# Optimization experiments

Hardware: AMD Instinct MI355X
Metric: run time of the kernel (lower is better)

## Reference

```python
import jax, jax.numpy as jnp
import numpy as np

NUM_HEADS = 12
HEAD_DIM = 64
SO3_DIM = 30  # round(64*0.5)//3*3
ROPE_FREQ = 100.0


def _rope1d(t, p):
    # t: [B,H,N,Dh], p: [B,N]
    half = t.shape[-1] // 2
    inv = 1.0 / (ROPE_FREQ ** (jnp.arange(half, dtype=jnp.float32) / half))
    ang = p[:, None, :, None] * inv  # [B,1,N,half]
    cos = jnp.concatenate([jnp.cos(ang)] * 2, axis=-1)
    sin = jnp.concatenate([jnp.sin(ang)] * 2, axis=-1)
    t1, t2 = t[..., :half], t[..., half:]
    return t * cos + jnp.concatenate([-t2, t1], axis=-1) * sin


def _rope2d(x, pos):
    # x: [B,H,N,D], pos: [B,N,2] (y,x)
    Dh = x.shape[-1] // 2
    return jnp.concatenate([
        _rope1d(x[..., :Dh], pos[..., 0]),
        _rope1d(x[..., Dh:], pos[..., 1]),
    ], axis=-1)


def _so3prope(t, R, num_img):
    # t: [B,H,S,Nt,Dh], R: [B,S,3,3]; rotate first SO3_DIM channels of the
    # first num_img (image) tokens as 3-vectors; special tokens untouched.
    img, sp = t[..., :num_img, :], t[..., num_img:, :]
    B, H, S, Ni, D = img.shape
    v = img[..., :SO3_DIM].reshape(B, H, S, Ni, SO3_DIM // 3, 3)
    v = jnp.einsum('bsij,bhsnkj->bhsnki', R, v).reshape(B, H, S, Ni, SO3_DIM)
    img = jnp.concatenate([v, img[..., SO3_DIM:]], axis=-1)
    return jnp.concatenate([img, sp], axis=-2)


def setup_inputs() -> dict:
    key = jax.random.key(0)
    ks = jax.random.split(key, 6)
    B, HW, S, Nt, C = 1, 576, 4, 577, 768
    G = 24  # 24x24 patch grid
    q_tokens = jax.random.normal(ks[0], (B, HW, C), dtype=jnp.float32)
    t_tokens = jax.random.normal(ks[1], (B, S, Nt, C), dtype=jnp.float32)
    yy, xx = jnp.meshgrid(jnp.arange(G, dtype=jnp.float32), jnp.arange(G, dtype=jnp.float32), indexing='ij')
    pos2d = jnp.broadcast_to(jnp.stack([yy, xx], axis=-1).reshape(1, HW, 2), (B, HW, 2))
    # random proper rotations via QR
    A = jax.random.normal(ks[2], (B, S, 3, 3), dtype=jnp.float32)
    Q, _ = jnp.linalg.qr(A)
    poses = jnp.tile(jnp.eye(4, dtype=jnp.float32), (B, S, 1, 1))
    template_poses = poses.at[:, :, :3, :3].set(Q)
    W_qkv = jax.random.normal(ks[3], (C, 3 * C), dtype=jnp.float32) * 0.02
    b_qkv = jnp.zeros((3 * C,), dtype=jnp.float32)
    W_proj = jax.random.normal(ks[4], (C, C), dtype=jnp.float32) * 0.02
    b_proj = jnp.zeros((C,), dtype=jnp.float32)
    return {'q_tokens': q_tokens, 't_tokens': t_tokens, 'pos2d': pos2d,
            'template_poses': template_poses, 'W_qkv': W_qkv, 'b_qkv': b_qkv,
            'W_proj': W_proj, 'b_proj': b_proj}


def reference(q_tokens, t_tokens, pos2d, template_poses, W_qkv, b_qkv, W_proj, b_proj):
    B, HW, C = q_tokens.shape
    S, Nt = t_tokens.shape[1], t_tokens.shape[2]
    x = jnp.concatenate([q_tokens, t_tokens.reshape(B, S * Nt, C)], axis=1)  # [B,N,C]
    N = x.shape[1]
    qkv = (x @ W_qkv + b_qkv).reshape(B, N, 3, NUM_HEADS, HEAD_DIM)
    q = jnp.transpose(qkv[:, :, 0], (0, 2, 1, 3))  # [B,H,N,d]
    k = jnp.transpose(qkv[:, :, 1], (0, 2, 1, 3))
    v = jnp.transpose(qkv[:, :, 2], (0, 2, 1, 3))
    # RoPE2D on query-image tokens only
    q = jnp.concatenate([_rope2d(q[:, :, :HW], pos2d), q[:, :, HW:]], axis=2)
    k = jnp.concatenate([_rope2d(k[:, :, :HW], pos2d), k[:, :, HW:]], axis=2)
    # SO3Prope on template image tokens
    R = template_poses[:, :, :3, :3]
    q_t = _so3prope(q[:, :, HW:].reshape(B, NUM_HEADS, S, Nt, HEAD_DIM), R, HW)
    k_t = _so3prope(k[:, :, HW:].reshape(B, NUM_HEADS, S, Nt, HEAD_DIM), R, HW)
    q = jnp.concatenate([q[:, :, :HW], q_t.reshape(B, NUM_HEADS, S * Nt, HEAD_DIM)], axis=2)
    k = jnp.concatenate([k[:, :, :HW], k_t.reshape(B, NUM_HEADS, S * Nt, HEAD_DIM)], axis=2)
    # SDPA (no mask, no dropout at eval)
    scale = HEAD_DIM ** -0.5
    attn = jax.nn.softmax(jnp.einsum('bhnd,bhmd->bhnm', q, k) * scale, axis=-1)
    out = jnp.einsum('bhnm,bhmd->bhnd', attn, v)
    out = jnp.transpose(out, (0, 2, 1, 3)).reshape(B, N, C)
    out = out @ W_proj + b_proj
    return out[:, :HW, :], out[:, HW:, :].reshape(B, S, Nt, C)
```

## Files before the change

### kernel.cpp

```cpp
#include <hip/hip_runtime.h>
#include <hip/hip_bf16.h>
#include <hip/hip_fp16.h>
#include <math.h>

#define N_TOK 2884
#define HW_IMG 576
#define NT_TOK 577
#define CDIM 768
#define NH 12
#define HD 64
#define QKV_COLS 2304
#define NVP 2944
#define NQT 46
#define LOG2E 1.44269504088896340736f

typedef float f32x4 __attribute__((ext_vector_type(4)));
typedef short bf16x8 __attribute__((ext_vector_type(8)));
typedef _Float16 f16x8 __attribute__((ext_vector_type(8)));
typedef unsigned short u16;
typedef unsigned short u16x8 __attribute__((ext_vector_type(8)));
typedef unsigned short u16x4 __attribute__((ext_vector_type(4)));

static __device__ __forceinline__ u16 f2bf(float f) {
    union { __hip_bfloat16 b; u16 u; } cv;
    cv.b = __float2bfloat16(f);
    return cv.u;
}
static __device__ __forceinline__ float bf2f(u16 h) {
    return __uint_as_float(((unsigned)h) << 16);
}
static __device__ __forceinline__ void split1(float f, u16& h, u16& l) {
    h = f2bf(f);
    l = f2bf(f - bf2f(h));
}
static __device__ __forceinline__ f16x8 as_f16x8(u16x8 u) {
    union { u16x8 u; f16x8 h; } c; c.u = u; return c.h;
}

__global__ __launch_bounds__(256)
void conv_x(const float* __restrict__ q, const float* __restrict__ t,
            u16* __restrict__ Xhi, u16* __restrict__ Xlo)
{
    const int i = (blockIdx.x * 256 + threadIdx.x) * 4;
    const int SPLIT = HW_IMG * CDIM;
    const float4 v = (i < SPLIT) ? *(const float4*)(q + i) : *(const float4*)(t + (i - SPLIT));
    u16x4 h, l;
    u16 hh, ll;
    split1(v.x, hh, ll); h[0] = hh; l[0] = ll;
    split1(v.y, hh, ll); h[1] = hh; l[1] = ll;
    split1(v.z, hh, ll); h[2] = hh; l[2] = ll;
    split1(v.w, hh, ll); h[3] = hh; l[3] = ll;
    *(u16x4*)(Xhi + i) = h;
    *(u16x4*)(Xlo + i) = l;
}

__global__ __launch_bounds__(256)
void conv_wT(const float* __restrict__ W, int ncols,
             u16* __restrict__ Thi, u16* __restrict__ Tlo)
{
    __shared__ float T[64][65];
    const int k0 = blockIdx.x * 64;
    const int n0 = blockIdx.y * 64;
    const int tid = threadIdx.x;
    {
        const int kr = tid >> 2, nch = (tid & 3) << 4;
        const float* src = W + (size_t)(k0 + kr) * ncols + n0 + nch;
        #pragma unroll
        for (int c = 0; c < 4; ++c) {
            const float4 f = *(const float4*)(src + c * 4);
            T[kr][nch + c * 4 + 0] = f.x;
            T[kr][nch + c * 4 + 1] = f.y;
            T[kr][nch + c * 4 + 2] = f.z;
            T[kr][nch + c * 4 + 3] = f.w;
        }
    }
    __syncthreads();
    const int nr = tid >> 2, kch = (tid & 3) << 4;
    u16x8 h0, h1, l0v, l1v;
    #pragma unroll
    for (int j = 0; j < 8; ++j) { u16 hh, ll; split1(T[kch + j][nr], hh, ll); h0[j] = hh; l0v[j] = ll; }
    #pragma unroll
    for (int j = 0; j < 8; ++j) { u16 hh, ll; split1(T[kch + 8 + j][nr], hh, ll); h1[j] = hh; l1v[j] = ll; }
    const size_t dst = (size_t)(n0 + nr) * CDIM + k0 + kch;
    *(u16x8*)(Thi + dst) = h0;     *(u16x8*)(Thi + dst + 8) = h1;
    *(u16x8*)(Tlo + dst) = l0v;    *(u16x8*)(Tlo + dst + 8) = l1v;
}

__global__ __launch_bounds__(256, 3)
void qkv_mfma(const u16* __restrict__ Xhi, const u16* __restrict__ Xlo,
              const u16* __restrict__ Whi, const u16* __restrict__ Wlo,
              const float* __restrict__ bqkv,
              const float* __restrict__ pos2d, const float* __restrict__ tposes,
              u16* __restrict__ Qhi, u16* __restrict__ Qlo,
              u16* __restrict__ Khi, u16* __restrict__ Klo,
              u16* __restrict__ Vthi)
{
    __shared__ __align__(16) char smem[49152];
    u16 (*Ah)[64] = (u16(*)[64])(smem);
    u16 (*Al)[64] = (u16(*)[64])(smem + 16384);
    u16 (*Bh)[64] = (u16(*)[64])(smem + 32768);
    u16 (*Bl)[64] = (u16(*)[64])(smem + 40960);
    float (*Ct)[65] = (float(*)[65])(smem);

    const int rb = blockIdx.x;
    const int cb = blockIdx.y;
    const int which = cb / NH;
    const int h = cb - which * NH;
    const int colbase = cb * 64;
    const int tid = threadIdx.x;
    const int w = tid >> 6, l = tid & 63;
    const int lr = l & 15, lg = l >> 4;

    const int sa_r = tid >> 1;
    const int sa_c = (tid & 1) << 5;
    int arow = rb * 128 + sa_r;
    if (arow >= N_TOK) arow = N_TOK - 1;
    const size_t abase = (size_t)arow * CDIM + sa_c;
    const int swa_ = (sa_r & 7) << 3;
    const int sb_r = tid >> 2;
    const int sb_c = (tid & 3) << 4;
    const size_t bbase = (size_t)(colbase + sb_r) * CDIM + sb_c;
    const int swb_ = (sb_r & 7) << 3;

    const int swf = (lr & 7) << 3;

    f32x4 acc[2][4];
    #pragma unroll
    for (int rf = 0; rf < 2; ++rf)
        #pragma unroll
        for (int i = 0; i < 4; ++i) acc[rf][i] = (f32x4){0.f, 0.f, 0.f, 0.f};

    for (int k0 = 0; k0 < CDIM; k0 += 64) {
        u16x8 a_h[4], a_l[4], b_h[2], b_l[2];
        #pragma unroll
        for (int c = 0; c < 4; ++c) {
            a_h[c] = *(const u16x8*)(Xhi + abase + k0 + c * 8);
            a_l[c] = *(const u16x8*)(Xlo + abase + k0 + c * 8);
        }
        #pragma unroll
        for (int c = 0; c < 2; ++c) {
            b_h[c] = *(const u16x8*)(Whi + bbase + k0 + c * 8);
            b_l[c] = *(const u16x8*)(Wlo + bbase + k0 + c * 8);
        }
        __syncthreads();
        #pragma unroll
        for (int c = 0; c < 4; ++c) {
            *(u16x8*)&Ah[sa_r][(sa_c + c * 8) ^ swa_] = a_h[c];
            *(u16x8*)&Al[sa_r][(sa_c + c * 8) ^ swa_] = a_l[c];
        }
        #pragma unroll
        for (int c = 0; c < 2; ++c) {
            *(u16x8*)&Bh[sb_r][(sb_c + c * 8) ^ swb_] = b_h[c];
            *(u16x8*)&Bl[sb_r][(sb_c + c * 8) ^ swb_] = b_l[c];
        }
        __syncthreads();
        #pragma unroll
        for (int ks = 0; ks < 2; ++ks) {
            const int koff = (ks * 32 + lg * 8) ^ swf;
            const bf16x8 ah0 = *(const bf16x8*)&Ah[w * 32 + lr][koff];
            const bf16x8 al0 = *(const bf16x8*)&Al[w * 32 + lr][koff];
            const bf16x8 ah1 = *(const bf16x8*)&Ah[w * 32 + 16 + lr][koff];
            const bf16x8 al1 = *(const bf16x8*)&Al[w * 32 + 16 + lr][koff];
            #pragma unroll
            for (int cbk = 0; cbk < 4; ++cbk) {
                const bf16x8 bh_ = *(const bf16x8*)&Bh[cbk * 16 + lr][koff];
                const bf16x8 bl_ = *(const bf16x8*)&Bl[cbk * 16 + lr][koff];
                acc[0][cbk] = __builtin_amdgcn_mfma_f32_16x16x32_bf16(ah0, bh_, acc[0][cbk], 0, 0, 0);
                acc[0][cbk] = __builtin_amdgcn_mfma_f32_16x16x32_bf16(ah0, bl_, acc[0][cbk], 0, 0, 0);
                acc[0][cbk] = __builtin_amdgcn_mfma_f32_16x16x32_bf16(al0, bh_, acc[0][cbk], 0, 0, 0);
                acc[1][cbk] = __builtin_amdgcn_mfma_f32_16x16x32_bf16(ah1, bh_, acc[1][cbk], 0, 0, 0);
                acc[1][cbk] = __builtin_amdgcn_mfma_f32_16x16x32_bf16(ah1, bl_, acc[1][cbk], 0, 0, 0);
                acc[1][cbk] = __builtin_amdgcn_mfma_f32_16x16x32_bf16(al1, bh_, acc[1][cbk], 0, 0, 0);
            }
        }
    }

    __syncthreads();
    #pragma unroll
    for (int rf = 0; rf < 2; ++rf)
        #pragma unroll
        for (int cbk = 0; cbk < 4; ++cbk)
            #pragma unroll
            for (int r = 0; r < 4; ++r)
                Ct[w * 32 + rf * 16 + lg * 4 + r][cbk * 16 + lr] =
                    acc[rf][cbk][r] + bqkv[colbase + cbk * 16 + lr];
    __syncthreads();

    if (which < 2) {
        #pragma unroll
        for (int it = 0; it < 2; ++it) {
            const int item = it * 256 + tid;
            const int er = item >> 2;
            const int eu = item & 3;
            const int n = rb * 128 + er;
            if (n < N_TOK) {
                float outv[16];
                const bool is_img = (n < HW_IMG);
                int ts = 0, tj = 0;
                if (!is_img) { const int m = n - HW_IMG; ts = m / NT_TOK; tj = m - ts * NT_TOK; }

                if (is_img) {
                    const float p = (eu < 2) ? pos2d[2 * n] : pos2d[2 * n + 1];
                    const bool lowhalf = ((eu & 1) == 0);
                    #pragma unroll
                    for (int dd = 0; dd < 16; ++dd) {
                        const int d = (eu << 4) + dd;
                        float sv, cv;
                        sincosf(p * expf((float)dd * -0.28782313662425574f), &sv, &cv);
                        const float rot = lowhalf ? -Ct[er][d + 16] : Ct[er][d - 16];
                        outv[dd] = Ct[er][d] * cv + rot * sv;
                    }
                } else if (tj < HW_IMG) {
                    #pragma unroll
                    for (int dd = 0; dd < 16; ++dd) {
                        const int d = (eu << 4) + dd;
                        float val = Ct[er][d];
                        if (d < 30) {
                            const int g = d / 3;
                            const float* R = tposes + ts * 16 + (d - g * 3) * 4;
                            val = R[0] * Ct[er][g * 3] + R[1] * Ct[er][g * 3 + 1] + R[2] * Ct[er][g * 3 + 2];
                        }
                        outv[dd] = val;
                    }
                } else {
                    #pragma unroll
                    for (int dd = 0; dd < 16; ++dd) outv[dd] = Ct[er][(eu << 4) + dd];
                }

                const float scale = (which == 0) ? (0.125f * LOG2E) : 1.0f;
                u16x8 h0, h1, l0v, l1v;
                #pragma unroll
                for (int j = 0; j < 8; ++j) { u16 hh, ll; split1(outv[j] * scale, hh, ll); h0[j] = hh; l0v[j] = ll; }
                #pragma unroll
                for (int j = 0; j < 8; ++j) { u16 hh, ll; split1(outv[8 + j] * scale, hh, ll); h1[j] = hh; l1v[j] = ll; }
                u16* dh = (which == 0 ? Qhi : Khi) + ((size_t)h * N_TOK + n) * HD + (eu << 4);
                u16* dl = (which == 0 ? Qlo : Klo) + ((size_t)h * N_TOK + n) * HD + (eu << 4);
                *(u16x8*)dh = h0;  *(u16x8*)(dh + 8) = h1;
                *(u16x8*)dl = l0v; *(u16x8*)(dl + 8) = l1v;
            }
        }
    } else {
        #pragma unroll
        for (int it = 0; it < 2; ++it) {
            const int item = it * 256 + tid;
            const int vd_ = item >> 3;
            const int vch = (item & 7) << 4;
            const int tokbase = rb * 128 + vch;
            u16 th[16];
            #pragma unroll
            for (int j = 0; j < 16; ++j)
                th[j] = (tokbase + j < N_TOK)
                      ? __half_as_ushort(__float2half(Ct[vch + j][vd_]))
                      : (u16)0;
            u16* dh = Vthi + (size_t)(h * HD + vd_) * NVP + tokbase;
            *(u16x8*)dh = *(u16x8*)&th[0];
            *(u16x8*)(dh + 8) = *(u16x8*)&th[8];
        }
    }
}

__global__ __launch_bounds__(256, 3)
void attn_shard(const u16* __restrict__ Qhi, const u16* __restrict__ Qlo,
                const u16* __restrict__ Khi, const u16* __restrict__ Klo,
                const u16* __restrict__ Vthi,
                float* __restrict__ Pacc, float2* __restrict__ PmL,
                int TS, int SPLITS)
{
    __shared__ __align__(16) u16 Kh_s[64][64], Kl_s[64][64];
    __shared__ __align__(16) u16 Vh_s[64][64];
    __shared__ __align__(16) u16 P2[64][64];

    int qb, head, sh;
    {
        const int flat = blockIdx.x + NQT * (blockIdx.y + NH * blockIdx.z);
        if (SPLITS == 4) {
            const int grp = flat & 7;
            const int rest = flat >> 3;
            qb = rest % NQT;
            const int hs = grp + 8 * (rest / NQT);
            head = hs % NH;
            sh = hs / NH;
        } else {
            qb = blockIdx.x; head = blockIdx.y; sh = blockIdx.z;
        }
    }
    const int tid = threadIdx.x;
    const int w = tid >> 6, l = tid & 63;
    const int lr = l & 15, lg = l >> 4;

    const int kt_begin = sh * TS;
    const int kt_end = min(NQT, kt_begin + TS);

    bf16x8 qh_[2], ql_[2];
    {
        int row = qb * 64 + w * 16 + lr;
        if (row >= N_TOK) row = N_TOK - 1;
        const u16* qph = Qhi + ((size_t)head * N_TOK + row) * HD;
        const u16* qpl = Qlo + ((size_t)head * N_TOK + row) * HD;
        #pragma unroll
        for (int ks = 0; ks < 2; ++ks) {
            qh_[ks] = *(const bf16x8*)(qph + ks * 32 + lg * 8);
            ql_[ks] = *(const bf16x8*)(qpl + ks * 32 + lg * 8);
        }
    }

    float m0[4] = {-1e30f, -1e30f, -1e30f, -1e30f};
    float l0[4] = {0.f, 0.f, 0.f, 0.f};
    f32x4 acc[4];
    #pragma unroll
    for (int db = 0; db < 4; ++db) acc[db] = (f32x4){0.f, 0.f, 0.f, 0.f};

    const int skey = tid >> 2, sch = (tid & 3) << 4;
    const int vd_ = tid >> 2, vch = (tid & 3) << 4;
    const int swk = (skey & 7) << 3;
    const int swv = (vd_ & 7) << 3;
    const int swf = (lr & 7) << 3;
    const u16* KhH = Khi + (size_t)head * N_TOK * HD;
    const u16* KlH = Klo + (size_t)head * N_TOK * HD;
    const size_t vrowbase = (size_t)(head * HD + vd_) * NVP;

    u16x8 rk0h, rk1h, rk0l, rk1l, rv0h, rv1h;
    auto LOADT = [&](int kt) {
        const int kbase = kt << 6;
        int krow = kbase + skey;
        if (krow >= N_TOK) krow = N_TOK - 1;
        const u16* kph = KhH + (size_t)krow * HD + sch;
        const u16* kpl = KlH + (size_t)krow * HD + sch;
        rk0h = *(const u16x8*)kph;  rk1h = *(const u16x8*)(kph + 8);
        rk0l = *(const u16x8*)kpl;  rk1l = *(const u16x8*)(kpl + 8);
        const u16* vph = Vthi + vrowbase + kbase + vch;
        rv0h = *(const u16x8*)vph;  rv1h = *(const u16x8*)(vph + 8);
    };
    LOADT(kt_begin);

    for (int kt = kt_begin; kt < kt_end; ++kt) {
        const int kbase = kt << 6;

        __syncthreads();
        *(u16x8*)&Kh_s[skey][(sch + 0) ^ swk] = rk0h;
        *(u16x8*)&Kh_s[skey][(sch + 8) ^ swk] = rk1h;
        *(u16x8*)&Kl_s[skey][(sch + 0) ^ swk] = rk0l;
        *(u16x8*)&Kl_s[skey][(sch + 8) ^ swk] = rk1l;
        *(u16x8*)&Vh_s[vd_][(vch + 0) ^ swv] = rv0h;
        *(u16x8*)&Vh_s[vd_][(vch + 8) ^ swv] = rv1h;
        if (kt + 1 < kt_end) LOADT(kt + 1);
        __syncthreads();

        f32x4 s[4];
        __builtin_amdgcn_s_setprio(1);
        #pragma unroll
        for (int kb = 0; kb < 4; ++kb) {
            s[kb] = (f32x4){0.f, 0.f, 0.f, 0.f};
            const int key = kb * 16 + lr;
            #pragma unroll
            for (int ks = 0; ks < 2; ++ks) {
                const int koff = (ks * 32 + lg * 8) ^ swf;
                const bf16x8 bh = *(const bf16x8*)&Kh_s[key][koff];
                const bf16x8 bl = *(const bf16x8*)&Kl_s[key][koff];
                s[kb] = __builtin_amdgcn_mfma_f32_16x16x32_bf16(qh_[ks], bh, s[kb], 0, 0, 0);
                s[kb] = __builtin_amdgcn_mfma_f32_16x16x32_bf16(qh_[ks], bl, s[kb], 0, 0, 0);
                s[kb] = __builtin_amdgcn_mfma_f32_16x16x32_bf16(ql_[ks], bh, s[kb], 0, 0, 0);
            }
        }
        __builtin_amdgcn_s_setprio(0);

        if (kbase + 64 > N_TOK) {
            #pragma unroll
            for (int kb = 0; kb < 4; ++kb)
                if (kbase + kb * 16 + lr >= N_TOK) {
                    #pragma unroll
                    for (int r = 0; r < 4; ++r) s[kb][r] = -1e30f;
                }
        }

        float mt[4];
        #pragma unroll
        for (int r = 0; r < 4; ++r)
            mt[r] = fmaxf(fmaxf(s[0][r], s[1][r]), fmaxf(s[2][r], s[3][r]));
        #pragma unroll
        for (int r = 0; r < 4; ++r) {
            mt[r] = fmaxf(mt[r], __shfl_xor(mt[r], 1));
            mt[r] = fmaxf(mt[r], __shfl_xor(mt[r], 2));
            mt[r] = fmaxf(mt[r], __shfl_xor(mt[r], 4));
            mt[r] = fmaxf(mt[r], __shfl_xor(mt[r], 8));
        }
        const bool newmax = __any((mt[0] > m0[0]) | (mt[1] > m0[1]) |
                                  (mt[2] > m0[2]) | (mt[3] > m0[3]));
        if (newmax) {
            float al[4];
            #pragma unroll
            for (int r = 0; r < 4; ++r) {
                const float mn = fmaxf(m0[r], mt[r]);
                al[r] = __builtin_amdgcn_exp2f(m0[r] - mn);
                m0[r] = mn;
            }
            #pragma unroll
            for (int r = 0; r < 4; ++r) l0[r] *= al[r];
            #pragma unroll
            for (int db = 0; db < 4; ++db)
                #pragma unroll
                for (int r = 0; r < 4; ++r) acc[db][r] *= al[r];
        }
        #pragma unroll
        for (int kb = 0; kb < 4; ++kb)
            #pragma unroll
            for (int r = 0; r < 4; ++r)
                s[kb][r] = __builtin_amdgcn_exp2f(s[kb][r] - m0[r]);
        #pragma unroll
        for (int r = 0; r < 4; ++r)
            l0[r] += s[0][r] + s[1][r] + s[2][r] + s[3][r];

        #pragma unroll
        for (int r = 0; r < 4; ++r) {
            const int rw = w * 16 + lg * 4 + r;
            const int swp = (rw & 7) << 3;
            #pragma unroll
            for (int kb = 0; kb < 4; ++kb)
                P2[rw][(kb * 16 + lr) ^ swp] = __half_as_ushort(__float2half(s[kb][r]));
        }

        const int arow = w * 16 + lr;
        const int swpa = (arow & 7) << 3;
        #pragma unroll
        for (int ks = 0; ks < 2; ++ks) {
            const int kb8 = ks * 32 + lg * 8;
            const f16x8 pa = as_f16x8(*(const u16x8*)&P2[arow][kb8 ^ swpa]);
            __builtin_amdgcn_s_setprio(1);
            #pragma unroll
            for (int db = 0; db < 4; ++db) {
                const int vr = db * 16 + lr;
                const f16x8 vh = as_f16x8(*(const u16x8*)&Vh_s[vr][kb8 ^ swf]);
                acc[db] = __builtin_amdgcn_mfma_f32_16x16x32_f16(pa, vh, acc[db], 0, 0, 0);
            }
            __builtin_amdgcn_s_setprio(0);
        }
    }

    #pragma unroll
    for (int r = 0; r < 4; ++r) {
        l0[r] += __shfl_xor(l0[r], 1);
        l0[r] += __shfl_xor(l0[r], 2);
        l0[r] += __shfl_xor(l0[r], 4);
        l0[r] += __shfl_xor(l0[r], 8);
    }
    const size_t pb = (((size_t)sh * NH + head) * NQT + qb) << 6;
    float* pout = Pacc + (pb << 6);
    #pragma unroll
    for (int r = 0; r < 4; ++r) {
        const int lrow = w * 16 + lg * 4 + r;
        #pragma unroll
        for (int db = 0; db < 4; ++db)
            pout[(size_t)lrow * 64 + db * 16 + lr] = acc[db][r];
        if (lr == 0)
            PmL[pb + lrow] = make_float2(m0[r], l0[r]);
    }
}

__global__ __launch_bounds__(256)
void attn_combine(const float* __restrict__ Pacc, const float2* __restrict__ PmL,
                  u16* __restrict__ Ohi, u16* __restrict__ Olo, int SPLITS)
{
    const int qb = blockIdx.x, h = blockIdx.y;
    const int tid = threadIdx.x;
    const int er = tid >> 2, eu = tid & 3;
    const int row = qb * 64 + er;
    if (row >= N_TOK) return;

    float ms[4], ls[4];
    float m = -1e30f;
    for (int s = 0; s < SPLITS; ++s) {
        const float2 p = PmL[((((size_t)s * NH + h) * NQT + qb) << 6) + er];
        ms[s] = p.x; ls[s] = p.y;
        m = fmaxf(m, p.x);
    }
    float L = 0.f, Ws[4];
    for (int s = 0; s < SPLITS; ++s) { Ws[s] = __builtin_amdgcn_exp2f(ms[s] - m); L += ls[s] * Ws[s]; }
    const float inv = 1.f / L;

    float o[16];
    #pragma unroll
    for (int j = 0; j < 16; ++j) o[j] = 0.f;
    for (int s = 0; s < SPLITS; ++s) {
        const float* src = Pacc + ((((((size_t)s * NH + h) * NQT + qb) << 6) + er) << 6) + (eu << 4);
        const float wgt = Ws[s];
        #pragma unroll
        for (int c = 0; c < 4; ++c) {
            const float4 f = *(const float4*)(src + c * 4);
            o[c * 4 + 0] += wgt * f.x;
            o[c * 4 + 1] += wgt * f.y;
            o[c * 4 + 2] += wgt * f.z;
            o[c * 4 + 3] += wgt * f.w;
        }
    }
    u16x8 h0, h1, l0v, l1v;
    #pragma unroll
    for (int j = 0; j < 8; ++j) { u16 hh, ll; split1(o[j] * inv, hh, ll); h0[j] = hh; l0v[j] = ll; }
    #pragma unroll
    for (int j = 0; j < 8; ++j) { u16 hh, ll; split1(o[8 + j] * inv, hh, ll); h1[j] = hh; l1v[j] = ll; }
    u16* dh = Ohi + (size_t)row * CDIM + h * HD + (eu << 4);
    u16* dl = Olo + (size_t)row * CDIM + h * HD + (eu << 4);
    *(u16x8*)dh = h0;  *(u16x8*)(dh + 8) = h1;
    *(u16x8*)dl = l0v; *(u16x8*)(dl + 8) = l1v;
}

__global__ __launch_bounds__(256)
void proj_mfma(const u16* __restrict__ Ahi, const u16* __restrict__ Alo,
               const u16* __restrict__ Whi, const u16* __restrict__ Wlo,
               const float* __restrict__ bp, float* __restrict__ out)
{
    __shared__ __align__(16) u16 Ah[64][64], Al[64][64], Bh[64][64], Bl[64][64];

    const int rb = blockIdx.x;
    const int colbase = blockIdx.y * 64;
    const int tid = threadIdx.x;
    const int w = tid >> 6, l = tid & 63;
    const int lr = l & 15, lg = l >> 4;

    const int srow = tid >> 2, sch = (tid & 3) << 4;
    int arow = rb * 64 + srow;
    if (arow >= N_TOK) arow = N_TOK - 1;
    const size_t abase = (size_t)arow * CDIM + sch;
    const size_t bbase = (size_t)(colbase + srow) * CDIM + sch;

    f32x4 acc[4];
    #pragma unroll
    for (int i = 0; i < 4; ++i) acc[i] = (f32x4){0.f, 0.f, 0.f, 0.f};

    const int sw = (srow & 7) << 3;
    const int swf = (lr & 7) << 3;

    for (int k0 = 0; k0 < CDIM; k0 += 64) {
        const u16x8 a0h = *(const u16x8*)(Ahi + abase + k0);
        const u16x8 a1h = *(const u16x8*)(Ahi + abase + k0 + 8);
        const u16x8 a0l = *(const u16x8*)(Alo + abase + k0);
        const u16x8 a1l = *(const u16x8*)(Alo + abase + k0 + 8);
        const u16x8 b0h = *(const u16x8*)(Whi + bbase + k0);
        const u16x8 b1h = *(const u16x8*)(Whi + bbase + k0 + 8);
        const u16x8 b0l = *(const u16x8*)(Wlo + bbase + k0);
        const u16x8 b1l = *(const u16x8*)(Wlo + bbase + k0 + 8);
        __syncthreads();
        *(u16x8*)&Ah[srow][(sch + 0) ^ sw] = a0h;
        *(u16x8*)&Ah[srow][(sch + 8) ^ sw] = a1h;
        *(u16x8*)&Al[srow][(sch + 0) ^ sw] = a0l;
        *(u16x8*)&Al[srow][(sch + 8) ^ sw] = a1l;
        *(u16x8*)&Bh[srow][(sch + 0) ^ sw] = b0h;
        *(u16x8*)&Bh[srow][(sch + 8) ^ sw] = b1h;
        *(u16x8*)&Bl[srow][(sch + 0) ^ sw] = b0l;
        *(u16x8*)&Bl[srow][(sch + 8) ^ sw] = b1l;
        __syncthreads();
        #pragma unroll
        for (int ks = 0; ks < 2; ++ks) {
            const int koff = (ks * 32 + lg * 8) ^ swf;
            const bf16x8 ah_ = *(const bf16x8*)&Ah[w * 16 + lr][koff];
            const bf16x8 al_ = *(const bf16x8*)&Al[w * 16 + lr][koff];
            #pragma unroll
            for (int cbk = 0; cbk < 4; ++cbk) {
                const bf16x8 bh_ = *(const bf16x8*)&Bh[cbk * 16 + lr][koff];
                const bf16x8 bl_ = *(const bf16x8*)&Bl[cbk * 16 + lr][koff];
                acc[cbk] = __builtin_amdgcn_mfma_f32_16x16x32_bf16(ah_, bh_, acc[cbk], 0, 0, 0);
                acc[cbk] = __builtin_amdgcn_mfma_f32_16x16x32_bf16(ah_, bl_, acc[cbk], 0, 0, 0);
                acc[cbk] = __builtin_amdgcn_mfma_f32_16x16x32_bf16(al_, bh_, acc[cbk], 0, 0, 0);
            }
        }
    }

    #pragma unroll
    for (int cbk = 0; cbk < 4; ++cbk) {
        const float bb = bp[colbase + cbk * 16 + lr];
        #pragma unroll
        for (int r = 0; r < 4; ++r) {
            const int row = rb * 64 + w * 16 + lg * 4 + r;
            if (row < N_TOK)
                out[(size_t)row * CDIM + colbase + cbk * 16 + lr] = acc[cbk][r] + bb;
        }
    }
}

extern "C" void kernel_launch(void* const* d_in, const int* in_sizes, int n_in,
                              void* d_out, int out_size, void* d_ws, size_t ws_size,
                              hipStream_t stream)
{
    const float* q_tokens = (const float*)d_in[0];
    const float* t_tokens = (const float*)d_in[1];
    const float* pos2d    = (const float*)d_in[2];
    const float* tposes   = (const float*)d_in[3];
    const float* Wqkv     = (const float*)d_in[4];
    const float* bqkv     = (const float*)d_in[5];
    const float* Wproj    = (const float*)d_in[6];
    const float* bproj    = (const float*)d_in[7];
    float* out = (float*)d_out;

    const size_t PQ = (size_t)NH * N_TOK * HD;
    const size_t PV_ = (size_t)NH * HD * NVP;
    const size_t PX = (size_t)N_TOK * CDIM;
    const size_t PW = (size_t)QKV_COLS * CDIM;

    u16* base = (u16*)d_ws;
    u16* Qhi  = base;
    u16* Qlo  = Qhi + PQ;
    u16* Khi  = Qlo + PQ;
    u16* Klo  = Khi + PQ;
    u16* Vthi = Klo + PQ;
    u16* XOhi = Vthi + PV_;
    u16* XOlo = XOhi + PX;
    u16* WThi = XOlo + PX;
    u16* WTlo = WThi + PW;
    u16* planes_end = WTlo + PW;

    const size_t planes_bytes = (size_t)(planes_end - base) * sizeof(u16);
    const size_t accElems = (size_t)NH * NQT * 64 * 64;
    const size_t mlElems  = (size_t)NH * NQT * 64;
    const size_t per_shard = accElems * 4 + mlElems * 8;

    int SPLITS = 1;
    for (int cand = 4; cand >= 2; --cand) {
        if (planes_bytes + (size_t)cand * per_shard <= ws_size) { SPLITS = cand; break; }
    }
    float* Pacc = (float*)((char*)d_ws + planes_bytes);
    float2* PmL = (float2*)(Pacc + (size_t)SPLITS * accElems);
    const int TS = (NQT + SPLITS - 1) / SPLITS;

    conv_x<<<dim3((N_TOK * CDIM / 4 + 255) / 256), 256, 0, stream>>>(q_tokens, t_tokens, XOhi, XOlo);
    conv_wT<<<dim3(CDIM / 64, QKV_COLS / 64), 256, 0, stream>>>(Wqkv, QKV_COLS, WThi, WTlo);

    dim3 g1((N_TOK + 127) / 128, 36);
    qkv_mfma<<<g1, 256, 0, stream>>>(XOhi, XOlo, WThi, WTlo, bqkv, pos2d, tposes,
                                     Qhi, Qlo, Khi, Klo, Vthi);

    conv_wT<<<dim3(CDIM / 64, CDIM / 64), 256, 0, stream>>>(Wproj, CDIM, WThi, WTlo);

    dim3 g2(NQT, NH, SPLITS);
    attn_shard<<<g2, 256, 0, stream>>>(Qhi, Qlo, Khi, Klo, Vthi, Pacc, PmL, TS, SPLITS);

    dim3 g2b(NQT, NH);
    attn_combine<<<g2b, 256, 0, stream>>>(Pacc, PmL, XOhi, XOlo, SPLITS);

    dim3 g3((N_TOK + 63) / 64, CDIM / 64);
    proj_mfma<<<g3, 256, 0, stream>>>(XOhi, XOlo, WThi, WTlo, bproj, out);
}
```

Measured before the change: 202.7 us.

## Load QKV GEMM fragments directly from global with register double-buffering

Removes the LDS staging of A and B tiles in the QKV projection GEMM. Each lane now loads its MFMA fragments straight from global memory, with two register fragment sets alternating so the next K step loads while the current one computes. This drops the per-step barriers and shared-memory traffic. The cost is redundant global loads (B rows are reread by all four waves, with no cross-wave reuse), uncoalesced 16-byte strided accesses, and higher register pressure under launch bounds of 3 blocks.

Result: slower. 269.2 us (+32.8%).

```diff
diff --git a/kernel.cpp b/kernel.cpp
--- a/kernel.cpp
+++ b/kernel.cpp
@@ -86,6 +86,11 @@
     *(u16x8*)(Tlo + dst) = l0v;    *(u16x8*)(Tlo + dst + 8) = l1v;
 }
 
+struct Frags {
+    bf16x8 a0h, a0l, a1h, a1l;
+    bf16x8 bh[4], bl[4];
+};
+
 __global__ __launch_bounds__(256, 3)
 void qkv_mfma(const u16* __restrict__ Xhi, const u16* __restrict__ Xlo,
               const u16* __restrict__ Whi, const u16* __restrict__ Wlo,
@@ -95,12 +100,7 @@
               u16* __restrict__ Khi, u16* __restrict__ Klo,
               u16* __restrict__ Vthi)
 {
-    __shared__ __align__(16) char smem[49152];
-    u16 (*Ah)[64] = (u16(*)[64])(smem);
-    u16 (*Al)[64] = (u16(*)[64])(smem + 16384);
-    u16 (*Bh)[64] = (u16(*)[64])(smem + 32768);
-    u16 (*Bl)[64] = (u16(*)[64])(smem + 40960);
-    float (*Ct)[65] = (float(*)[65])(smem);
+    __shared__ float Ct[128][65];
 
     const int rb = blockIdx.x;
     const int cb = blockIdx.y;
@@ -111,18 +111,13 @@
     const int w = tid >> 6, l = tid & 63;
     const int lr = l & 15, lg = l >> 4;
 
-    const int sa_r = tid >> 1;
-    const int sa_c = (tid & 1) << 5;
-    int arow = rb * 128 + sa_r;
-    if (arow >= N_TOK) arow = N_TOK - 1;
-    const size_t abase = (size_t)arow * CDIM + sa_c;
-    const int swa_ = (sa_r & 7) << 3;
-    const int sb_r = tid >> 2;
-    const int sb_c = (tid & 3) << 4;
-    const size_t bbase = (size_t)(colbase + sb_r) * CDIM + sb_c;
-    const int swb_ = (sb_r & 7) << 3;
-
-    const int swf = (lr & 7) << 3;
+    int ar0 = rb * 128 + w * 32 + lr;       if (ar0 >= N_TOK) ar0 = N_TOK - 1;
+    int ar1 = rb * 128 + w * 32 + 16 + lr;  if (ar1 >= N_TOK) ar1 = N_TOK - 1;
+    const u16* pA0h = Xhi + (size_t)ar0 * CDIM + lg * 8;
+    const u16* pA0l = Xlo + (size_t)ar0 * CDIM + lg * 8;
+    const u16* pA1h = Xhi + (size_t)ar1 * CDIM + lg * 8;
+    const u16* pA1l = Xlo + (size_t)ar1 * CDIM + lg * 8;
+    const size_t brow = (size_t)(colbase + lr) * CDIM + lg * 8;
 
     f32x4 acc[2][4];
     #pragma unroll
@@ -130,52 +125,42 @@
         #pragma unroll
         for (int i = 0; i < 4; ++i) acc[rf][i] = (f32x4){0.f, 0.f, 0.f, 0.f};
 
-    for (int k0 = 0; k0 < CDIM; k0 += 64) {
-        u16x8 a_h[4], a_l[4], b_h[2], b_l[2];
-        #pragma unroll
-        for (int c = 0; c < 4; ++c) {
-            a_h[c] = *(const u16x8*)(Xhi + abase + k0 + c * 8);
-            a_l[c] = *(const u16x8*)(Xlo + abase + k0 + c * 8);
-        }
-        #pragma unroll
-        for (int c = 0; c < 2; ++c) {
-            b_h[c] = *(const u16x8*)(Whi + bbase + k0 + c * 8);
-            b_l[c] = *(const u16x8*)(Wlo + bbase + k0 + c * 8);
-        }
-        __syncthreads();
-        #pragma unroll
-        for (int c = 0; c < 4; ++c) {
-            *(u16x8*)&Ah[sa_r][(sa_c + c * 8) ^ swa_] = a_h[c];
-            *(u16x8*)&Al[sa_r][(sa_c + c * 8) ^ swa_] = a_l[c];
-        }
-        #pragma unroll
-        for (int c = 0; c < 2; ++c) {
-            *(u16x8*)&Bh[sb_r][(sb_c + c * 8) ^ swb_] = b_h[c];
-            *(u16x8*)&Bl[sb_r][(sb_c + c * 8) ^ swb_] = b_l[c];
-        }
-        __syncthreads();
-        #pragma unroll
-        for (int ks = 0; ks < 2; ++ks) {
-            const int koff = (ks * 32 + lg * 8) ^ swf;
-            const bf16x8 ah0 = *(const bf16x8*)&Ah[w * 32 + lr][koff];
-            const bf16x8 al0 = *(const bf16x8*)&Al[w * 32 + lr][koff];
-            const bf16x8 ah1 = *(const bf16x8*)&Ah[w * 32 + 16 + lr][koff];
-            const bf16x8 al1 = *(const bf16x8*)&Al[w * 32 + 16 + lr][koff];
-            #pragma unroll
-            for (int cbk = 0; cbk < 4; ++cbk) {
-                const bf16x8 bh_ = *(const bf16x8*)&Bh[cbk * 16 + lr][koff];
-                const bf16x8 bl_ = *(const bf16x8*)&Bl[cbk * 16 + lr][koff];
-                acc[0][cbk] = __builtin_amdgcn_mfma_f32_16x16x32_bf16(ah0, bh_, acc[0][cbk], 0, 0, 0);
-                acc[0][cbk] = __builtin_amdgcn_mfma_f32_16x16x32_bf16(ah0, bl_, acc[0][cbk], 0, 0, 0);
-                acc[0][cbk] = __builtin_amdgcn_mfma_f32_16x16x32_bf16(al0, bh_, acc[0][cbk], 0, 0, 0);
-                acc[1][cbk] = __builtin_amdgcn_mfma_f32_16x16x32_bf16(ah1, bh_, acc[1][cbk], 0, 0, 0);
-                acc[1][cbk] = __builtin_amdgcn_mfma_f32_16x16x32_bf16(ah1, bl_, acc[1][cbk], 0, 0, 0);
-                acc[1][cbk] = __builtin_amdgcn_mfma_f32_16x16x32_bf16(al1, bh_, acc[1][cbk], 0, 0, 0);
-            }
-        }
-    }
-
-    __syncthreads();
+    Frags fr0, fr1;
+    #define LDSTEP(FR, STEP) do {                                               \
+        const int ko_ = (STEP) * 32;                                            \
+        (FR).a0h = *(const bf16x8*)(pA0h + ko_);                                \
+        (FR).a0l = *(const bf16x8*)(pA0l + ko_);                                \
+        (FR).a1h = *(const bf16x8*)(pA1h + ko_);                                \
+        (FR).a1l = *(const bf16x8*)(pA1l + ko_);                                \
+        _Pragma("unroll")                                                       \
+        for (int c_ = 0; c_ < 4; ++c_) {                                        \
+            (FR).bh[c_] = *(const bf16x8*)(Whi + brow + (size_t)c_ * 16 * CDIM + ko_); \
+            (FR).bl[c_] = *(const bf16x8*)(Wlo + brow + (size_t)c_ * 16 * CDIM + ko_); \
+        }                                                                       \
+    } while (0)
+    #define CPSTEP(FR) do {                                                     \
+        _Pragma("unroll")                                                       \
+        for (int c_ = 0; c_ < 4; ++c_) {                                        \
+            acc[0][c_] = __builtin_amdgcn_mfma_f32_16x16x32_bf16((FR).a0h, (FR).bh[c_], acc[0][c_], 0, 0, 0); \
+            acc[0][c_] = __builtin_amdgcn_mfma_f32_16x16x32_bf16((FR).a0h, (FR).bl[c_], acc[0][c_], 0, 0, 0); \
+            acc[0][c_] = __builtin_amdgcn_mfma_f32_16x16x32_bf16((FR).a0l, (FR).bh[c_], acc[0][c_], 0, 0, 0); \
+            acc[1][c_] = __builtin_amdgcn_mfma_f32_16x16x32_bf16((FR).a1h, (FR).bh[c_], acc[1][c_], 0, 0, 0); \
+            acc[1][c_] = __builtin_amdgcn_mfma_f32_16x16x32_bf16((FR).a1h, (FR).bl[c_], acc[1][c_], 0, 0, 0); \
+            acc[1][c_] = __builtin_amdgcn_mfma_f32_16x16x32_bf16((FR).a1l, (FR).bh[c_], acc[1][c_], 0, 0, 0); \
+        }                                                                       \
+    } while (0)
+
+    LDSTEP(fr0, 0);
+    #pragma unroll
+    for (int it = 0; it < 12; ++it) {
+        LDSTEP(fr1, 2 * it + 1);
+        CPSTEP(fr0);
+        if (it < 11) LDSTEP(fr0, 2 * it + 2);
+        CPSTEP(fr1);
+    }
+    #undef LDSTEP
+    #undef CPSTEP
+
     #pragma unroll
     for (int rf = 0; rf < 2; ++rf)
         #pragma unroll
```

## Fuse split-attention combine into output projection GEMM A-tile load

Applied to the files above, without the earlier changes.

Removes the separate attn_combine kernel. The projection GEMM now reads the per-split partial accumulators and max/sum stats directly, merges them, normalizes, splits into hi/lo bf16 and writes the A tile to shared memory. This saves one launch and a round trip of the bf16 hi/lo attention output through global memory. In exchange, each of the 12 column blocks redoes the combine for the same rows, so fp32 partial reads and exp work are repeated twelve-fold.

Result: slower. 222.4 us (+9.7%).

```diff
diff --git a/kernel.cpp b/kernel.cpp
--- a/kernel.cpp
+++ b/kernel.cpp
@@ -457,56 +457,9 @@
 }
 
 __global__ __launch_bounds__(256)
-void attn_combine(const float* __restrict__ Pacc, const float2* __restrict__ PmL,
-                  u16* __restrict__ Ohi, u16* __restrict__ Olo, int SPLITS)
-{
-    const int qb = blockIdx.x, h = blockIdx.y;
-    const int tid = threadIdx.x;
-    const int er = tid >> 2, eu = tid & 3;
-    const int row = qb * 64 + er;
-    if (row >= N_TOK) return;
-
-    float ms[4], ls[4];
-    float m = -1e30f;
-    for (int s = 0; s < SPLITS; ++s) {
-        const float2 p = PmL[((((size_t)s * NH + h) * NQT + qb) << 6) + er];
-        ms[s] = p.x; ls[s] = p.y;
-        m = fmaxf(m, p.x);
-    }
-    float L = 0.f, Ws[4];
-    for (int s = 0; s < SPLITS; ++s) { Ws[s] = __builtin_amdgcn_exp2f(ms[s] - m); L += ls[s] * Ws[s]; }
-    const float inv = 1.f / L;
-
-    float o[16];
-    #pragma unroll
-    for (int j = 0; j < 16; ++j) o[j] = 0.f;
-    for (int s = 0; s < SPLITS; ++s) {
-        const float* src = Pacc + ((((((size_t)s * NH + h) * NQT + qb) << 6) + er) << 6) + (eu << 4);
-        const float wgt = Ws[s];
-        #pragma unroll
-        for (int c = 0; c < 4; ++c) {
-            const float4 f = *(const float4*)(src + c * 4);
-            o[c * 4 + 0] += wgt * f.x;
-            o[c * 4 + 1] += wgt * f.y;
-            o[c * 4 + 2] += wgt * f.z;
-            o[c * 4 + 3] += wgt * f.w;
-        }
-    }
-    u16x8 h0, h1, l0v, l1v;
-    #pragma unroll
-    for (int j = 0; j < 8; ++j) { u16 hh, ll; split1(o[j] * inv, hh, ll); h0[j] = hh; l0v[j] = ll; }
-    #pragma unroll
-    for (int j = 0; j < 8; ++j) { u16 hh, ll; split1(o[8 + j] * inv, hh, ll); h1[j] = hh; l1v[j] = ll; }
-    u16* dh = Ohi + (size_t)row * CDIM + h * HD + (eu << 4);
-    u16* dl = Olo + (size_t)row * CDIM + h * HD + (eu << 4);
-    *(u16x8*)dh = h0;  *(u16x8*)(dh + 8) = h1;
-    *(u16x8*)dl = l0v; *(u16x8*)(dl + 8) = l1v;
-}
-
-__global__ __launch_bounds__(256)
-void proj_mfma(const u16* __restrict__ Ahi, const u16* __restrict__ Alo,
-               const u16* __restrict__ Whi, const u16* __restrict__ Wlo,
-               const float* __restrict__ bp, float* __restrict__ out)
+void proj_fused(const float* __restrict__ Pacc, const float2* __restrict__ PmL,
+                const u16* __restrict__ Whi, const u16* __restrict__ Wlo,
+                const float* __restrict__ bp, float* __restrict__ out, int SPLITS)
 {
     __shared__ __align__(16) u16 Ah[64][64], Al[64][64], Bh[64][64], Bl[64][64];
 
@@ -517,10 +470,8 @@
     const int lr = l & 15, lg = l >> 4;
 
     const int srow = tid >> 2, sch = (tid & 3) << 4;
-    int arow = rb * 64 + srow;
-    if (arow >= N_TOK) arow = N_TOK - 1;
-    const size_t abase = (size_t)arow * CDIM + sch;
-    const size_t bbase = (size_t)(colbase + srow) * CDIM + sch;
+    const int sb_r = tid >> 2, sb_c = (tid & 3) << 4;
+    const size_t bbase = (size_t)(colbase + sb_r) * CDIM + sb_c;
 
     f32x4 acc[4];
     #pragma unroll
@@ -530,24 +481,60 @@
     const int swf = (lr & 7) << 3;
 
     for (int k0 = 0; k0 < CDIM; k0 += 64) {
-        const u16x8 a0h = *(const u16x8*)(Ahi + abase + k0);
-        const u16x8 a1h = *(const u16x8*)(Ahi + abase + k0 + 8);
-        const u16x8 a0l = *(const u16x8*)(Alo + abase + k0);
-        const u16x8 a1l = *(const u16x8*)(Alo + abase + k0 + 8);
+        const int h = k0 >> 6;
+
         const u16x8 b0h = *(const u16x8*)(Whi + bbase + k0);
         const u16x8 b1h = *(const u16x8*)(Whi + bbase + k0 + 8);
         const u16x8 b0l = *(const u16x8*)(Wlo + bbase + k0);
         const u16x8 b1l = *(const u16x8*)(Wlo + bbase + k0 + 8);
+
+        float ms[4], ls[4];
+        float m = -1e30f;
+        #pragma unroll
+        for (int s = 0; s < 4; ++s)
+            if (s < SPLITS) {
+                const float2 p = PmL[((((size_t)s * NH + h) * NQT + rb) << 6) + srow];
+                ms[s] = p.x; ls[s] = p.y;
+                m = fmaxf(m, p.x);
+            }
+        float L = 0.f, Wsv[4];
+        #pragma unroll
+        for (int s = 0; s < 4; ++s)
+            if (s < SPLITS) { Wsv[s] = __builtin_amdgcn_exp2f(ms[s] - m); L += ls[s] * Wsv[s]; }
+        const float inv = 1.f / L;
+
+        float o[16];
+        #pragma unroll
+        for (int j = 0; j < 16; ++j) o[j] = 0.f;
+        #pragma unroll
+        for (int s = 0; s < 4; ++s)
+            if (s < SPLITS) {
+                const float* src = Pacc + (((((size_t)s * NH + h) * NQT + rb) << 6) + srow) * 64 + sch;
+                const float wgt = Wsv[s];
+                #pragma unroll
+                for (int c = 0; c < 4; ++c) {
+                    const float4 f = *(const float4*)(src + c * 4);
+                    o[c * 4 + 0] += wgt * f.x;
+                    o[c * 4 + 1] += wgt * f.y;
+                    o[c * 4 + 2] += wgt * f.z;
+                    o[c * 4 + 3] += wgt * f.w;
+                }
+            }
+        u16 ahv[16], alv[16];
+        #pragma unroll
+        for (int j = 0; j < 16; ++j) { u16 hh, ll; split1(o[j] * inv, hh, ll); ahv[j] = hh; alv[j] = ll; }
+
         __syncthreads();
-        *(u16x8*)&Ah[srow][(sch + 0) ^ sw] = a0h;
-        *(u16x8*)&Ah[srow][(sch + 8) ^ sw] = a1h;
-        *(u16x8*)&Al[srow][(sch + 0) ^ sw] = a0l;
-        *(u16x8*)&Al[srow][(sch + 8) ^ sw] = a1l;
-        *(u16x8*)&Bh[srow][(sch + 0) ^ sw] = b0h;
-        *(u16x8*)&Bh[srow][(sch + 8) ^ sw] = b1h;
-        *(u16x8*)&Bl[srow][(sch + 0) ^ sw] = b0l;
-        *(u16x8*)&Bl[srow][(sch + 8) ^ sw] = b1l;
+        *(u16x8*)&Ah[srow][(sch + 0) ^ sw] = *(u16x8*)&ahv[0];
+        *(u16x8*)&Ah[srow][(sch + 8) ^ sw] = *(u16x8*)&ahv[8];
+        *(u16x8*)&Al[srow][(sch + 0) ^ sw] = *(u16x8*)&alv[0];
+        *(u16x8*)&Al[srow][(sch + 8) ^ sw] = *(u16x8*)&alv[8];
+        *(u16x8*)&Bh[sb_r][(sb_c + 0) ^ sw] = b0h;
+        *(u16x8*)&Bh[sb_r][(sb_c + 8) ^ sw] = b1h;
+        *(u16x8*)&Bl[sb_r][(sb_c + 0) ^ sw] = b0l;
+        *(u16x8*)&Bl[sb_r][(sb_c + 8) ^ sw] = b1l;
         __syncthreads();
+
         #pragma unroll
         for (int ks = 0; ks < 2; ++ks) {
             const int koff = (ks * 32 + lg * 8) ^ swf;
@@ -632,9 +619,6 @@
     dim3 g2(NQT, NH, SPLITS);
     attn_shard<<<g2, 256, 0, stream>>>(Qhi, Qlo, Khi, Klo, Vthi, Pacc, PmL, TS, SPLITS);
 
-    dim3 g2b(NQT, NH);
-    attn_combine<<<g2b, 256, 0, stream>>>(Pacc, PmL, XOhi, XOlo, SPLITS);
-
     dim3 g3((N_TOK + 63) / 64, CDIM / 64);
-    proj_mfma<<<g3, 256, 0, stream>>>(XOhi, XOlo, WThi, WTlo, bproj, out);
-}
+    proj_fused<<<g3, 256, 0, stream>>>(Pacc, PmL, WThi, WTlo, bproj, out, SPLITS);
+}
```
